# Optimization experiments

Measured on AMD Instinct MI355X. Metric: run time of the kernel, lower is better.

The kernel has to match this reference:

```python
import jax, jax.numpy as jnp
import numpy as np

DEPTH = 2
DIM = 512
FF = 2048
INNER = 32
VOCAB = 8192
B = 2
L = 512
LN_EPS = 1e-5


def _layer_norm(x, g, b):
    m = jnp.mean(x, axis=-1, keepdims=True)
    v = jnp.var(x, axis=-1, keepdims=True)
    return (x - m) * jax.lax.rsqrt(v + LN_EPS) * g + b


def _sioconv_layer(x, wa, wx, v_re, v_im, h0_re, h0_im, w_ol):
    # x: [B, L, DIM] float32
    Bb, Ll, _ = x.shape
    I = v_re.shape[0]
    # complex gate a with magnitude sigmoid(log|a|^2)
    af = (x @ wa.T).reshape(Bb, Ll, I, 2)
    a = jax.lax.complex(af[..., 0], af[..., 1])
    m = jnp.square(af[..., 0]) + jnp.square(af[..., 1])
    a = a * jax.lax.rsqrt(m) * jax.nn.sigmoid(jnp.log(m))  # [B,L,I] complex
    # complex input x with magnitude |x| (x * rsqrt(|x|^2) * |x|^2)
    xf = (x @ wx.T).reshape(Bb, Ll, I, 2)
    xc = jax.lax.complex(xf[..., 0], xf[..., 1])
    mx = jnp.square(xf[..., 0]) + jnp.square(xf[..., 1])
    xc = xc * jax.lax.rsqrt(mx) * mx  # [B,L,I] complex
    # cumulative log-decay products: the original's FFT conv of the upper-
    # triangular a_ln against an all-ones matrix is exactly a cumsum along j.
    a_ln = jnp.log(a)  # [B,L,I]
    ii = jnp.arange(Ll)[:, None]
    jj = jnp.arange(Ll)[None, :]
    tri = jnp.where((jj >= ii)[None, None, :, :],
                    jnp.transpose(a_ln, (0, 2, 1))[:, :, None, :],
                    jnp.zeros((), a_ln.dtype))  # [B,I,L,L]: tri[b,d,i,j]=a_ln[b,j,d] for j>=i
    s = jnp.cumsum(tri, axis=3)
    # c[b,d,i,j] = prod_{t=i..j} a[b,t,d] for j>=i; =1 at j=i-1; 0 below.
    c = jnp.where((jj >= ii - 1)[None, None, :, :], jnp.exp(s), jnp.zeros((), s.dtype))
    V = jax.lax.complex(v_re, v_im)
    Vinv = jnp.linalg.inv(V)
    h0 = jax.lax.complex(h0_re, h0_im)  # [I]
    xct = jnp.transpose(xc, (0, 2, 1))  # [B,I,L]
    x_roll = jnp.roll(xct, 1, axis=2).at[:, :, 0].set(h0[None, :])
    # original builds C[b,l,m,n,o] = V diag(c) V^-1 then einsum; contract lazily:
    y = jnp.einsum('ko,bol->bkl', Vinv, x_roll)  # eigenbasis inputs [B,I,L]
    t = jnp.einsum('bkij,bki->bjk', c, y)        # recurrence in eigenbasis [B,L,I]
    h = jnp.einsum('bjk,nk->bjn', t, V)          # back to state basis [B,L,I]
    h = h.at[:, -1, :].add(xc[:, -1, :])         # last step input (others already in c via j=i-1 band)
    return jnp.real(h) @ w_ol.T


def setup_inputs() -> dict:
    key = jax.random.key(0)
    ks = jax.random.split(key, 16)
    f = lambda k, shp: jax.random.normal(k, shp, dtype=jnp.float32)
    return {
        'x': f(ks[0], (B, L, VOCAB)),
        'w_in': f(ks[1], (DIM, VOCAB)) * VOCAB ** -0.5,
        'b_in': jnp.zeros((DIM,), jnp.float32),
        'ln1_g': jnp.ones((DEPTH, DIM), jnp.float32),
        'ln1_b': jnp.zeros((DEPTH, DIM), jnp.float32),
        'wa': f(ks[2], (DEPTH, 2 * INNER, DIM)) * DIM ** -0.5,
        'wx': f(ks[3], (DEPTH, 2 * INNER, DIM)) * DIM ** -0.5,
        'v_re': f(ks[4], (DEPTH, INNER, INNER)),
        'v_im': f(ks[5], (DEPTH, INNER, INNER)),
        'h0_re': f(ks[6], (DEPTH, INNER)),
        'h0_im': f(ks[7], (DEPTH, INNER)),
        'w_ol': f(ks[8], (DEPTH, DIM, INNER)) * INNER ** -0.5,
        'ln2_g': jnp.ones((DEPTH, DIM), jnp.float32),
        'ln2_b': jnp.zeros((DEPTH, DIM), jnp.float32),
        'w1': f(ks[9], (DEPTH, FF, DIM)) * DIM ** -0.5,
        'b1': jnp.zeros((DEPTH, FF), jnp.float32),
        'w2': f(ks[10], (DEPTH, DIM, FF)) * FF ** -0.5,
        'b2': jnp.zeros((DEPTH, DIM), jnp.float32),
        'lnl_g': jnp.ones((DIM,), jnp.float32),
        'lnl_b': jnp.zeros((DIM,), jnp.float32),
        'w_out': f(ks[11], (VOCAB, DIM)) * DIM ** -0.5,
        'b_out': jnp.zeros((VOCAB,), jnp.float32),
    }


def reference(x, w_in, b_in, ln1_g, ln1_b, wa, wx, v_re, v_im, h0_re, h0_im,
              w_ol, ln2_g, ln2_b, w1, b1, w2, b2, lnl_g, lnl_b, w_out, b_out):
    h = x @ w_in.T + b_in  # [B,L,DIM]
    for d in range(DEPTH):
        r = h
        z = _layer_norm(h, ln1_g[d], ln1_b[d])
        z = _sioconv_layer(z, wa[d], wx[d], v_re[d], v_im[d], h0_re[d], h0_im[d], w_ol[d])
        h = z + r
        r = h
        z = _layer_norm(h, ln2_g[d], ln2_b[d])
        z = jax.nn.silu(z @ w1[d].T + b1[d]) @ w2[d].T + b2[d]
        h = z + r
    h = _layer_norm(h, lnl_g, lnl_b)
    return h @ w_out.T + b_out
```

## Files before the change

### kernel.cpp

```cpp
#include <hip/hip_runtime.h>
#include <stdint.h>

#define DEPTHC 2
#define DIMC   512
#define FFC    2048
#define INNERC 32
#define VOCABC 8192
#define BC     2
#define LC     512
#define NTOK   1024

typedef _Float16 f16;
typedef __attribute__((ext_vector_type(8))) _Float16 f16x8;
typedef __attribute__((ext_vector_type(4))) float f32x4;

__device__ __forceinline__ float2 cmul2(float2 a, float2 b){
    return make_float2(a.x*b.x - a.y*b.y, a.x*b.y + a.y*b.x);
}
__device__ __forceinline__ float2 cadd2(float2 a, float2 b){
    return make_float2(a.x + b.x, a.y + b.y);
}

__device__ __forceinline__ void gl_lds16(const void* g, void* l){
    __builtin_amdgcn_global_load_lds(
        (const __attribute__((address_space(1))) unsigned int*)g,
        (__attribute__((address_space(3))) unsigned int*)l, 16, 0, 0);
}

__global__ __launch_bounds__(256) void k_prep(
    const float* __restrict__ s0, const float* __restrict__ s1,
    const float* __restrict__ s2, const float* __restrict__ s3,
    const float* __restrict__ s4,
    f16* __restrict__ d0, f16* __restrict__ d1, f16* __restrict__ d2,
    f16* __restrict__ d3, f16* __restrict__ d4,
    int n0, int n1, int n2, int n3, int n4,
    const float* __restrict__ v_re, const float* __restrict__ v_im,
    const float* __restrict__ h0re, const float* __restrict__ h0im,
    float2* __restrict__ vinv, float2* __restrict__ h0c)
{
    __shared__ float2 M[32][64];
    if (blockIdx.x < 2){
        const int d = blockIdx.x;
        const int tid = threadIdx.x;
        const int c = tid & 63;
        const int wv = tid >> 6;
        if (tid < 32) h0c[d*32 + tid] = make_float2(h0re[d*32 + tid], h0im[d*32 + tid]);
#pragma unroll
        for (int rr = 0; rr < 8; ++rr){
            int r = wv*8 + rr;
            float re, im;
            if (c < 32){ re = v_re[d*1024 + r*32 + c]; im = v_im[d*1024 + r*32 + c]; }
            else       { re = (c - 32 == r) ? 1.f : 0.f; im = 0.f; }
            M[r][c] = make_float2(re, im);
        }
        __syncthreads();
#pragma unroll 1
        for (int col = 0; col < 32; ++col){
            float2 prow = M[col][c];
            float pvx = __shfl(prow.x, col, 64);
            float pvy = __shfl(prow.y, col, 64);
            float dm = pvx*pvx + pvy*pvy;
            float ir = pvx/dm, ii = -pvy/dm;
            float2 nv = make_float2(prow.x*ir - prow.y*ii, prow.x*ii + prow.y*ir);
#pragma unroll
            for (int rr = 0; rr < 8; ++rr){
                int r = wv*8 + rr;
                if (r == col) continue;
                float2 f  = M[r][col];
                float2 m0 = M[r][c];
                m0.x -= f.x*nv.x - f.y*nv.y;
                m0.y -= f.x*nv.y + f.y*nv.x;
                M[r][c] = m0;
            }
            __syncthreads();
        }
        if (c >= 32){
#pragma unroll
            for (int rr = 0; rr < 8; ++rr){
                int r = wv*8 + rr;
                float2 dv = M[r][r];
                float dm = dv.x*dv.x + dv.y*dv.y;
                float ir = dv.x/dm, ii = -dv.y/dm;
                float2 m0 = M[r][c];
                vinv[d*1024 + r*32 + (c - 32)] =
                    make_float2(m0.x*ir - m0.y*ii, m0.x*ii + m0.y*ir);
            }
        }
        return;
    }
    long long i = ((long long)(blockIdx.x - 2) * 256 + threadIdx.x) * 4;
    const float* s; f16* d;
    if (i < n0){ s = s0; d = d0; }
    else { i -= n0;
        if (i < n1){ s = s1; d = d1; }
        else { i -= n1;
            if (i < n2){ s = s2; d = d2; }
            else { i -= n2;
                if (i < n3){ s = s3; d = d3; }
                else { i -= n3; if (i >= n4) return; s = s4; d = d4; }
            }
        }
    }
    float4 v = *(const float4*)(s + i);
    union { f16 h[4]; float2 f2; } u;
    u.h[0] = (f16)v.x; u.h[1] = (f16)v.y; u.h[2] = (f16)v.z; u.h[3] = (f16)v.w;
    *(float2*)(d + i) = u.f2;
}

template<int MT, int NT, int MODE>
__global__ __launch_bounds__(256) void k_gemmT(
    const f16* __restrict__ A, const f16* __restrict__ Bw,
    void* __restrict__ C, const float* __restrict__ bias,
    int N, int K, int klen, int partStride)
{
    constexpr int RM = MT/32, RN = NT/32;
    __shared__ __align__(16) f16 As[MT*64];
    __shared__ __align__(16) f16 Bs[NT*64];
    const int tid = threadIdx.x;
    const int m0 = blockIdx.y * MT;
    const int n0 = blockIdx.x * NT;
    const int kbeg = blockIdx.z * klen;
    const int l = tid & 63;
    const int w = tid >> 6;
    const int fr = l & 15;
    const int fq = l >> 4;
    const int wm = (w >> 1) * (MT/2);
    const int wn = (w & 1) * (NT/2);
    const f16* gA = A  + (size_t)(m0 + (tid >> 3)) * K + kbeg + (tid & 7) * 8;
    const f16* gB = Bw + (size_t)(n0 + (tid >> 3)) * K + kbeg + (tid & 7) * 8;
    const size_t rowskip = (size_t)32 * K;
    f16* lA = As + tid * 8;
    f16* lB = Bs + tid * 8;
    f32x4 acc[RM][RN];
#pragma unroll
    for (int i = 0; i < RM; ++i)
#pragma unroll
        for (int j = 0; j < RN; ++j)
            acc[i][j] = (f32x4){0.f, 0.f, 0.f, 0.f};
    for (int kk = 0; kk < klen; kk += 64){
        __syncthreads();
#pragma unroll
        for (int i = 0; i < MT/32; ++i) gl_lds16(gA + i*rowskip, lA + i*2048);
#pragma unroll
        for (int i = 0; i < NT/32; ++i) gl_lds16(gB + i*rowskip, lB + i*2048);
        gA += 64; gB += 64;
        __syncthreads();
#pragma unroll
        for (int h = 0; h < 2; ++h){
            f16x8 af[RM], bf[RN];
#pragma unroll
            for (int i = 0; i < RM; ++i) af[i] = *(const f16x8*)(As + (wm + 16*i + fr) * 64 + h*32 + fq * 8);
#pragma unroll
            for (int j = 0; j < RN; ++j) bf[j] = *(const f16x8*)(Bs + (wn + 16*j + fr) * 64 + h*32 + fq * 8);
#pragma unroll
            for (int i = 0; i < RM; ++i)
#pragma unroll
                for (int j = 0; j < RN; ++j)
                    acc[i][j] = __builtin_amdgcn_mfma_f32_16x16x32_f16(af[i], bf[j], acc[i][j], 0, 0, 0);
        }
    }
#pragma unroll
    for (int i = 0; i < RM; ++i)
#pragma unroll
        for (int j = 0; j < RN; ++j)
#pragma unroll
            for (int r = 0; r < 4; ++r){
                int row = m0 + wm + 16*i + fq*4 + r;
                int col = n0 + wn + 16*j + fr;
                if (MODE == 1){
                    ((f16*)C + (size_t)blockIdx.z * partStride)[(size_t)row * N + col] = (f16)acc[i][j][r];
                } else if (MODE == 0){
                    ((float*)C)[(size_t)row * N + col] = acc[i][j][r] + bias[col];
                } else {
                    float v = acc[i][j][r] + bias[col];
                    ((f16*)C)[(size_t)row * N + col] = (f16)(v / (1.f + __expf(-v)));
                }
            }
}

__global__ __launch_bounds__(128) void k_red8_ln(
    const f16* __restrict__ part, const float* __restrict__ bias,
    const float* __restrict__ res, const float* __restrict__ g,
    const float* __restrict__ b, f16* __restrict__ out, int n)
{
    int row = blockIdx.x;
    int tid = threadIdx.x;
    __shared__ float sw[2], qw[2];
    float v[4]; float s = 0.f, q = 0.f;
#pragma unroll
    for (int j = 0; j < 4; ++j){
        int c = tid + 128*j;
        int idx = row*DIMC + c;
        float t = bias[c] + res[idx];
#pragma unroll
        for (int z = 0; z < 8; ++z) t += (float)part[(size_t)z * n + idx];
        v[j] = t; s += t; q += t*t;
    }
    for (int off = 32; off; off >>= 1){ s += __shfl_down(s, off, 64); q += __shfl_down(q, off, 64); }
    if ((tid & 63) == 0){ sw[tid >> 6] = s; qw[tid >> 6] = q; }
    __syncthreads();
    float S = sw[0] + sw[1], Q = qw[0] + qw[1];
    float m = S / DIMC;
    float rstd = rsqrtf(Q / DIMC - m*m + 1e-5f);
#pragma unroll
    for (int j = 0; j < 4; ++j){
        int c = tid + 128*j;
        out[(size_t)row*DIMC + c] = (f16)((v[j] - m)*rstd*g[c] + b[c]);
    }
}

__global__ __launch_bounds__(128) void k_siogate(
    const f16* __restrict__ part, const float* __restrict__ bias0,
    const float* __restrict__ res, float* __restrict__ hout,
    const float* __restrict__ g, const float* __restrict__ b,
    const float* __restrict__ wa, const float* __restrict__ wx,
    float2* __restrict__ a_t, float2* __restrict__ xc)
{
    __shared__ float zs[4][DIMC];
    __shared__ float sc[4][128];
    __shared__ float rs2[2], rq2[2];
    int tid = threadIdx.x;
    int r0 = blockIdx.x * 4;
    for (int gg = 0; gg < 4; ++gg){
        int row = r0 + gg;
        float v[4]; float s = 0.f, q = 0.f;
#pragma unroll
        for (int j = 0; j < 4; ++j){
            int c = tid + 128*j;
            size_t idx = (size_t)row * DIMC + c;
            float t = bias0[c];
            if (res) t += res[idx];
#pragma unroll
            for (int z = 0; z < 8; ++z) t += (float)part[(size_t)z * (NTOK*DIMC) + idx];
            hout[idx] = t;
            v[j] = t; s += t; q += t*t;
        }
        for (int off = 32; off; off >>= 1){ s += __shfl_down(s, off, 64); q += __shfl_down(q, off, 64); }
        if ((tid & 63) == 0){ rs2[tid >> 6] = s; rq2[tid >> 6] = q; }
        __syncthreads();
        float m = (rs2[0] + rs2[1]) / DIMC;
        float var = (rq2[0] + rq2[1]) / DIMC - m*m;
        float rst = rsqrtf(var + 1e-5f);
#pragma unroll
        for (int j = 0; j < 4; ++j){ int c = tid + 128*j; zs[gg][c] = (v[j] - m)*rst*g[c] + b[c]; }
        __syncthreads();
    }
    const float* wrow = (tid < 64) ? (wa + (size_t)tid * DIMC) : (wx + (size_t)(tid - 64) * DIMC);
    float dot[4] = {0.f, 0.f, 0.f, 0.f};
    for (int c = 0; c < DIMC; c += 4){
        float4 wv = *(const float4*)(wrow + c);
#pragma unroll
        for (int gg = 0; gg < 4; ++gg){
            float4 zv = *(const float4*)(&zs[gg][c]);
            dot[gg] += wv.x*zv.x + wv.y*zv.y + wv.z*zv.z + wv.w*zv.w;
        }
    }
#pragma unroll
    for (int gg = 0; gg < 4; ++gg) sc[gg][tid] = dot[gg];
    __syncthreads();
    int gg = tid >> 5, k = tid & 31;
    int row = r0 + gg;
    int bb = row >> 9, t = row & 511;
    float re = sc[gg][2*k], im = sc[gg][2*k + 1];
    float m2 = re*re + im*im;
    float sa = rsqrtf(m2) * (m2 / (1.f + m2));
    a_t[(size_t)(bb*INNERC + k)*LC + t] = make_float2(re*sa, im*sa);
    float xr2 = sc[gg][64 + 2*k], xi2 = sc[gg][64 + 2*k + 1];
    float mx = xr2*xr2 + xi2*xi2;
    float sx = sqrtf(mx);
    xc[(size_t)row*INNERC + k] = make_float2(xr2*sx, xi2*sx);
}

__global__ __launch_bounds__(64) void k_scan(
    const float2* __restrict__ a_t, const float2* __restrict__ xc,
    const float2* __restrict__ vinv, const float2* __restrict__ h0c,
    float2* __restrict__ e)
{
    int bk = blockIdx.x;
    int l = threadIdx.x;
    int bb = bk >> 5, k = bk & 31;
    float2 vrow[32];
#pragma unroll
    for (int o = 0; o < 32; ++o) vrow[o] = vinv[k*32 + o];
    int base = bk * LC + l * 8;
    float2 av[8], wv[8];
#pragma unroll
    for (int j = 0; j < 8; ++j) av[j] = a_t[base + j];
#pragma unroll
    for (int j = 0; j < 8; ++j){
        int t = l*8 + j;
        const float2* src = (t == 0) ? h0c : (xc + (size_t)(bb*LC + t - 1) * INNERC);
        float2 acc = make_float2(0.f, 0.f);
#pragma unroll
        for (int o = 0; o < 32; o += 2){
            float4 qq = *(const float4*)(src + o);
            acc.x += vrow[o].x*qq.x - vrow[o].y*qq.y;
            acc.y += vrow[o].x*qq.y + vrow[o].y*qq.x;
            acc.x += vrow[o+1].x*qq.z - vrow[o+1].y*qq.w;
            acc.y += vrow[o+1].x*qq.w + vrow[o+1].y*qq.z;
        }
        wv[j] = acc;
    }
    float2 A = make_float2(1.f, 0.f), Bc = make_float2(0.f, 0.f);
#pragma unroll
    for (int j = 0; j < 8; ++j){
        Bc = cmul2(av[j], cadd2(Bc, wv[j]));
        A  = cmul2(av[j], A);
    }
    for (int off = 1; off < 64; off <<= 1){
        float Apx = __shfl_up(A.x,  off, 64), Apy = __shfl_up(A.y,  off, 64);
        float Bpx = __shfl_up(Bc.x, off, 64), Bpy = __shfl_up(Bc.y, off, 64);
        if (l >= off){
            float2 Ap = make_float2(Apx, Apy), Bp = make_float2(Bpx, Bpy);
            Bc = cadd2(cmul2(A, Bp), Bc);
            A  = cmul2(A, Ap);
        }
    }
    float ex = __shfl_up(Bc.x, 1, 64), ey = __shfl_up(Bc.y, 1, 64);
    float2 ecur = (l == 0) ? make_float2(0.f, 0.f) : make_float2(ex, ey);
    size_t obase = ((size_t)bb*LC + l*8) * INNERC + k;
#pragma unroll
    for (int j = 0; j < 8; ++j){
        ecur = cmul2(av[j], cadd2(ecur, wv[j]));
        e[obase + (size_t)j * INNERC] = ecur;
    }
}

__global__ __launch_bounds__(128) void k_siout_ln(
    const float2* __restrict__ e, const float2* __restrict__ xc,
    const float* __restrict__ vre, const float* __restrict__ vim,
    const float* __restrict__ wol, const float* __restrict__ res,
    const float* __restrict__ g2, const float* __restrict__ b2,
    float* __restrict__ hout, f16* __restrict__ zout)
{
    int bt = blockIdx.x;
    int tid = threadIdx.x;
    __shared__ float hr[INNERC];
    __shared__ float2 er[INNERC];
    __shared__ float sw[2], qw[2];
    if (tid < 32) er[tid] = e[(size_t)bt*INNERC + tid];
    __syncthreads();
    if (tid < 32){
        const float* vrr = vre + tid*INNERC;
        const float* vir = vim + tid*INNERC;
        float acc = xc[(size_t)bt*INNERC + tid].x;
#pragma unroll
        for (int k2 = 0; k2 < 32; ++k2) acc += vrr[k2]*er[k2].x - vir[k2]*er[k2].y;
        hr[tid] = acc;
    }
    __syncthreads();
    float v[4]; float s = 0.f, q = 0.f;
#pragma unroll
    for (int j = 0; j < 4; ++j){
        int n = tid + 128*j;
        float val = res[(size_t)bt*DIMC + n];
        const float* wr = wol + (size_t)n * INNERC;
#pragma unroll
        for (int i = 0; i < 32; ++i) val += hr[i]*wr[i];
        hout[(size_t)bt*DIMC + n] = val;
        v[j] = val; s += val; q += val*val;
    }
    for (int off = 32; off; off >>= 1){ s += __shfl_down(s, off, 64); q += __shfl_down(q, off, 64); }
    if ((tid & 63) == 0){ sw[tid >> 6] = s; qw[tid >> 6] = q; }
    __syncthreads();
    float S = sw[0] + sw[1], Q = qw[0] + qw[1];
    float m = S / DIMC;
    float rstd = rsqrtf(Q / DIMC - m*m + 1e-5f);
#pragma unroll
    for (int j = 0; j < 4; ++j){
        int n = tid + 128*j;
        zout[(size_t)bt*DIMC + n] = (f16)((v[j] - m)*rstd*g2[n] + b2[n]);
    }
}

extern "C" void kernel_launch(void* const* d_in, const int* in_sizes, int n_in,
                              void* d_out, int out_size, void* d_ws, size_t ws_size,
                              hipStream_t stream)
{
    const float* x     = (const float*)d_in[0];
    const float* w_in  = (const float*)d_in[1];
    const float* b_in  = (const float*)d_in[2];
    const float* ln1_g = (const float*)d_in[3];
    const float* ln1_b = (const float*)d_in[4];
    const float* wa    = (const float*)d_in[5];
    const float* wx    = (const float*)d_in[6];
    const float* v_re  = (const float*)d_in[7];
    const float* v_im  = (const float*)d_in[8];
    const float* h0_re = (const float*)d_in[9];
    const float* h0_im = (const float*)d_in[10];
    const float* w_ol  = (const float*)d_in[11];
    const float* ln2_g = (const float*)d_in[12];
    const float* ln2_b = (const float*)d_in[13];
    const float* w1    = (const float*)d_in[14];
    const float* b1    = (const float*)d_in[15];
    const float* w2    = (const float*)d_in[16];
    const float* b2    = (const float*)d_in[17];
    const float* lnl_g = (const float*)d_in[18];
    const float* lnl_b = (const float*)d_in[19];
    const float* w_out = (const float*)d_in[20];
    const float* b_out = (const float*)d_in[21];

    char* p = (char*)d_ws;
    f16* xb   = (f16*)p;   p += (size_t)NTOK * VOCABC * 2;
    f16* wib  = (f16*)p;   p += (size_t)DIMC * VOCABC * 2;
    f16* wob  = (f16*)p;   p += (size_t)VOCABC * DIMC * 2;
    f16* w1b  = (f16*)p;   p += (size_t)DEPTHC * FFC * DIMC * 2;
    f16* w2b  = (f16*)p;   p += (size_t)DEPTHC * DIMC * FFC * 2;
    float* h1 = (float*)p; p += (size_t)NTOK * DIMC * 4;
    float* h2 = (float*)p; p += (size_t)NTOK * DIMC * 4;
    float* h3 = (float*)p; p += (size_t)NTOK * DIMC * 4;
    f16* zb   = (f16*)p;   p += (size_t)NTOK * DIMC * 2;
    f16* ffb  = (f16*)p;   p += (size_t)NTOK * FFC * 2;
    f16* pbuf = (f16*)p;   p += (size_t)8 * NTOK * DIMC * 2;
    float2* a_t = (float2*)p; p += (size_t)BC * INNERC * LC * 8;
    float2* xc  = (float2*)p; p += (size_t)NTOK * INNERC * 8;
    float2* ev  = (float2*)p; p += (size_t)NTOK * INNERC * 8;
    float2* vinv = (float2*)p; p += (size_t)DEPTHC * INNERC * INNERC * 8;
    float2* h0c  = (float2*)p; p += (size_t)DEPTHC * INNERC * 8;

    {
        const int n0 = NTOK*VOCABC, n1 = DIMC*VOCABC, n2 = DEPTHC*FFC*DIMC,
                  n3 = DEPTHC*DIMC*FFC, n4 = VOCABC*DIMC;
        int blocks = (n0 + n1 + n2 + n3 + n4) / 1024 + 2;
        k_prep<<<blocks, 256, 0, stream>>>(x, w_in, w1, w2, w_out,
                                           xb, wib, w1b, w2b, wob, n0, n1, n2, n3, n4,
                                           v_re, v_im, h0_re, h0_im, vinv, h0c);
    }

    {
        dim3 g(DIMC/128, NTOK/128, 8);
        k_gemmT<128,128,1><<<g, 256, 0, stream>>>(xb, wib, pbuf, nullptr, DIMC, VOCABC, VOCABC/8, NTOK*DIMC);
    }

    for (int d = 0; d < DEPTHC; ++d){
        float* cur = (d == 0) ? h1 : h3;
        float* hb  = h2;
        const float* redBias = (d == 0) ? b_in : (b2 + (d-1)*DIMC);
        const float* redRes  = (d == 0) ? nullptr : h2;
        k_siogate<<<NTOK/4, 128, 0, stream>>>(pbuf, redBias, redRes, cur,
                                              ln1_g + d*DIMC, ln1_b + d*DIMC,
                                              wa + (size_t)d*2*INNERC*DIMC,
                                              wx + (size_t)d*2*INNERC*DIMC, a_t, xc);
        k_scan<<<BC*INNERC, 64, 0, stream>>>(a_t, xc, vinv + d*INNERC*INNERC, h0c + d*INNERC, ev);
        k_siout_ln<<<NTOK, 128, 0, stream>>>(ev, xc, v_re + d*INNERC*INNERC, v_im + d*INNERC*INNERC,
                                             w_ol + (size_t)d*DIMC*INNERC, cur,
                                             ln2_g + d*DIMC, ln2_b + d*DIMC, hb, zb);
        {
            dim3 g(FFC/128, NTOK/64, 1);
            k_gemmT<64,128,2><<<g, 256, 0, stream>>>(zb, w1b + (size_t)d*FFC*DIMC, ffb, b1 + d*FFC,
                                                     FFC, DIMC, DIMC, 0);
        }
        {
            dim3 g(DIMC/128, NTOK/64, 8);
            k_gemmT<64,128,1><<<g, 256, 0, stream>>>(ffb, w2b + (size_t)d*DIMC*FFC, pbuf, nullptr,
                                                     DIMC, FFC, FFC/8, NTOK*DIMC);
        }
    }
    k_red8_ln<<<NTOK, 128, 0, stream>>>(pbuf, b2 + (DEPTHC-1)*DIMC, h2, lnl_g, lnl_b, zb, NTOK*DIMC);
    {
        dim3 g(VOCABC/128, NTOK/128, 1);
        k_gemmT<128,128,0><<<g, 256, 0, stream>>>(zb, wob, (float*)d_out, b_out, VOCABC, DIMC, DIMC, 0);
    }
    (void)in_sizes; (void)n_in; (void)out_size; (void)ws_size;
}
```

Baseline: 378.1 us.

## Move SioConv gate projection onto MFMA GEMM with fused complex-gate epilogue

Replaces the fused LayerNorm-plus-scalar-dot-product gate kernel with a separate LayerNorm kernel followed by an fp16 MFMA GEMM (new MODE 3). The GEMM epilogue pairs real and imaginary lanes via a shuffle and computes the a and x complex gates. The wa/wx weights are converted to fp16 in the prep kernel. The input projection GEMM tile also changes from 128x128 to 64x128 to launch more blocks. This trades an extra launch and round trip through global memory for tensor-core throughput, and gate inputs now go through fp16.

```diff
diff --git a/kernel.cpp b/kernel.cpp
--- a/kernel.cpp
+++ b/kernel.cpp
@@ -31,8 +31,9 @@
     const float* __restrict__ s0, const float* __restrict__ s1,
     const float* __restrict__ s2, const float* __restrict__ s3,
     const float* __restrict__ s4,
+    const float* __restrict__ wa4, const float* __restrict__ wx4,
     f16* __restrict__ d0, f16* __restrict__ d1, f16* __restrict__ d2,
-    f16* __restrict__ d3, f16* __restrict__ d4,
+    f16* __restrict__ d3, f16* __restrict__ d4, f16* __restrict__ wgb,
     int n0, int n1, int n2, int n3, int n4,
     const float* __restrict__ v_re, const float* __restrict__ v_im,
     const float* __restrict__ h0re, const float* __restrict__ h0im,
@@ -97,7 +98,27 @@
             if (i < n2){ s = s2; d = d2; }
             else { i -= n2;
                 if (i < n3){ s = s3; d = d3; }
-                else { i -= n3; if (i >= n4) return; s = s4; d = d4; }
+                else { i -= n3;
+                    if (i < n4){ s = s4; d = d4; }
+                    else {
+                        i -= n4;
+                        if (i >= 131072) return;
+                        const float* gs; f16* gd;
+                        if (i < 65536){
+                            int dd = (int)(i >> 15), rem = (int)(i & 32767);
+                            gs = wa4 + i; gd = wgb + dd*65536 + rem;
+                        } else {
+                            long long e2 = i - 65536;
+                            int dd = (int)(e2 >> 15), rem = (int)(e2 & 32767);
+                            gs = wx4 + e2; gd = wgb + dd*65536 + 32768 + rem;
+                        }
+                        float4 v = *(const float4*)gs;
+                        union { f16 h[4]; float2 f2; } u;
+                        u.h[0] = (f16)v.x; u.h[1] = (f16)v.y; u.h[2] = (f16)v.z; u.h[3] = (f16)v.w;
+                        *(float2*)gd = u.f2;
+                        return;
+                    }
+                }
             }
         }
     }
@@ -111,7 +132,8 @@
 __global__ __launch_bounds__(256) void k_gemmT(
     const f16* __restrict__ A, const f16* __restrict__ Bw,
     void* __restrict__ C, const float* __restrict__ bias,
-    int N, int K, int klen, int partStride)
+    int N, int K, int klen, int partStride,
+    float2* __restrict__ a_tp, float2* __restrict__ xcp)
 {
     constexpr int RM = MT/32, RN = NT/32;
     __shared__ __align__(16) f16 As[MT*64];
@@ -171,17 +193,35 @@
                     ((f16*)C + (size_t)blockIdx.z * partStride)[(size_t)row * N + col] = (f16)acc[i][j][r];
                 } else if (MODE == 0){
                     ((float*)C)[(size_t)row * N + col] = acc[i][j][r] + bias[col];
-                } else {
+                } else if (MODE == 2){
                     float v = acc[i][j][r] + bias[col];
                     ((f16*)C)[(size_t)row * N + col] = (f16)(v / (1.f + __expf(-v)));
+                } else {
+                    float val = acc[i][j][r];
+                    float pv = __shfl_xor(val, 1, 64);
+                    if (!(fr & 1)){
+                        float re = val, im = pv;
+                        int bb = row >> 9, t = row & 511;
+                        float m2 = re*re + im*im;
+                        if (col < 64){
+                            int k = col >> 1;
+                            float sa = rsqrtf(m2) * (m2 / (1.f + m2));
+                            a_tp[(size_t)(bb*INNERC + k)*LC + t] = make_float2(re*sa, im*sa);
+                        } else {
+                            int k = (col - 64) >> 1;
+                            float sx = sqrtf(m2);
+                            xcp[(size_t)row*INNERC + k] = make_float2(re*sx, im*sx);
+                        }
+                    }
                 }
             }
 }
 
-__global__ __launch_bounds__(128) void k_red8_ln(
+__global__ __launch_bounds__(128) void k_ln1(
     const f16* __restrict__ part, const float* __restrict__ bias,
     const float* __restrict__ res, const float* __restrict__ g,
-    const float* __restrict__ b, f16* __restrict__ out, int n)
+    const float* __restrict__ b, f16* __restrict__ out,
+    float* __restrict__ hout, int n)
 {
     int row = blockIdx.x;
     int tid = threadIdx.x;
@@ -191,9 +231,11 @@
     for (int j = 0; j < 4; ++j){
         int c = tid + 128*j;
         int idx = row*DIMC + c;
-        float t = bias[c] + res[idx];
+        float t = bias[c];
+        if (res) t += res[idx];
 #pragma unroll
         for (int z = 0; z < 8; ++z) t += (float)part[(size_t)z * n + idx];
+        if (hout) hout[idx] = t;
         v[j] = t; s += t; q += t*t;
     }
     for (int off = 32; off; off >>= 1){ s += __shfl_down(s, off, 64); q += __shfl_down(q, off, 64); }
@@ -207,68 +249,6 @@
         int c = tid + 128*j;
         out[(size_t)row*DIMC + c] = (f16)((v[j] - m)*rstd*g[c] + b[c]);
     }
-}
-
-__global__ __launch_bounds__(128) void k_siogate(
-    const f16* __restrict__ part, const float* __restrict__ bias0,
-    const float* __restrict__ res, float* __restrict__ hout,
-    const float* __restrict__ g, const float* __restrict__ b,
-    const float* __restrict__ wa, const float* __restrict__ wx,
-    float2* __restrict__ a_t, float2* __restrict__ xc)
-{
-    __shared__ float zs[4][DIMC];
-    __shared__ float sc[4][128];
-    __shared__ float rs2[2], rq2[2];
-    int tid = threadIdx.x;
-    int r0 = blockIdx.x * 4;
-    for (int gg = 0; gg < 4; ++gg){
-        int row = r0 + gg;
-        float v[4]; float s = 0.f, q = 0.f;
-#pragma unroll
-        for (int j = 0; j < 4; ++j){
-            int c = tid + 128*j;
-            size_t idx = (size_t)row * DIMC + c;
-            float t = bias0[c];
-            if (res) t += res[idx];
-#pragma unroll
-            for (int z = 0; z < 8; ++z) t += (float)part[(size_t)z * (NTOK*DIMC) + idx];
-            hout[idx] = t;
-            v[j] = t; s += t; q += t*t;
-        }
-        for (int off = 32; off; off >>= 1){ s += __shfl_down(s, off, 64); q += __shfl_down(q, off, 64); }
-        if ((tid & 63) == 0){ rs2[tid >> 6] = s; rq2[tid >> 6] = q; }
-        __syncthreads();
-        float m = (rs2[0] + rs2[1]) / DIMC;
-        float var = (rq2[0] + rq2[1]) / DIMC - m*m;
-        float rst = rsqrtf(var + 1e-5f);
-#pragma unroll
-        for (int j = 0; j < 4; ++j){ int c = tid + 128*j; zs[gg][c] = (v[j] - m)*rst*g[c] + b[c]; }
-        __syncthreads();
-    }
-    const float* wrow = (tid < 64) ? (wa + (size_t)tid * DIMC) : (wx + (size_t)(tid - 64) * DIMC);
-    float dot[4] = {0.f, 0.f, 0.f, 0.f};
-    for (int c = 0; c < DIMC; c += 4){
-        float4 wv = *(const float4*)(wrow + c);
-#pragma unroll
-        for (int gg = 0; gg < 4; ++gg){
-            float4 zv = *(const float4*)(&zs[gg][c]);
-            dot[gg] += wv.x*zv.x + wv.y*zv.y + wv.z*zv.z + wv.w*zv.w;
-        }
-    }
-#pragma unroll
-    for (int gg = 0; gg < 4; ++gg) sc[gg][tid] = dot[gg];
-    __syncthreads();
-    int gg = tid >> 5, k = tid & 31;
-    int row = r0 + gg;
-    int bb = row >> 9, t = row & 511;
-    float re = sc[gg][2*k], im = sc[gg][2*k + 1];
-    float m2 = re*re + im*im;
-    float sa = rsqrtf(m2) * (m2 / (1.f + m2));
-    a_t[(size_t)(bb*INNERC + k)*LC + t] = make_float2(re*sa, im*sa);
-    float xr2 = sc[gg][64 + 2*k], xi2 = sc[gg][64 + 2*k + 1];
-    float mx = xr2*xr2 + xi2*xi2;
-    float sx = sqrtf(mx);
-    xc[(size_t)row*INNERC + k] = make_float2(xr2*sx, xi2*sx);
 }
 
 __global__ __launch_bounds__(64) void k_scan(
@@ -406,6 +386,7 @@
     f16* wob  = (f16*)p;   p += (size_t)VOCABC * DIMC * 2;
     f16* w1b  = (f16*)p;   p += (size_t)DEPTHC * FFC * DIMC * 2;
     f16* w2b  = (f16*)p;   p += (size_t)DEPTHC * DIMC * FFC * 2;
+    f16* wgb  = (f16*)p;   p += (size_t)DEPTHC * 2*INNERC*2 * DIMC * 2;
     float* h1 = (float*)p; p += (size_t)NTOK * DIMC * 4;
     float* h2 = (float*)p; p += (size_t)NTOK * DIMC * 4;
     float* h3 = (float*)p; p += (size_t)NTOK * DIMC * 4;
@@ -421,15 +402,17 @@
     {
         const int n0 = NTOK*VOCABC, n1 = DIMC*VOCABC, n2 = DEPTHC*FFC*DIMC,
                   n3 = DEPTHC*DIMC*FFC, n4 = VOCABC*DIMC;
-        int blocks = (n0 + n1 + n2 + n3 + n4) / 1024 + 2;
-        k_prep<<<blocks, 256, 0, stream>>>(x, w_in, w1, w2, w_out,
-                                           xb, wib, w1b, w2b, wob, n0, n1, n2, n3, n4,
+        int blocks = (n0 + n1 + n2 + n3 + n4 + 131072) / 1024 + 2;
+        k_prep<<<blocks, 256, 0, stream>>>(x, w_in, w1, w2, w_out, wa, wx,
+                                           xb, wib, w1b, w2b, wob, wgb,
+                                           n0, n1, n2, n3, n4,
                                            v_re, v_im, h0_re, h0_im, vinv, h0c);
     }
 
     {
-        dim3 g(DIMC/128, NTOK/128, 8);
-        k_gemmT<128,128,1><<<g, 256, 0, stream>>>(xb, wib, pbuf, nullptr, DIMC, VOCABC, VOCABC/8, NTOK*DIMC);
+        dim3 g(DIMC/128, NTOK/64, 8);
+        k_gemmT<64,128,1><<<g, 256, 0, stream>>>(xb, wib, pbuf, nullptr, DIMC, VOCABC, VOCABC/8, NTOK*DIMC,
+                                                 nullptr, nullptr);
     }
 
     for (int d = 0; d < DEPTHC; ++d){
@@ -437,10 +420,13 @@
         float* hb  = h2;
         const float* redBias = (d == 0) ? b_in : (b2 + (d-1)*DIMC);
         const float* redRes  = (d == 0) ? nullptr : h2;
-        k_siogate<<<NTOK/4, 128, 0, stream>>>(pbuf, redBias, redRes, cur,
-                                              ln1_g + d*DIMC, ln1_b + d*DIMC,
-                                              wa + (size_t)d*2*INNERC*DIMC,
-                                              wx + (size_t)d*2*INNERC*DIMC, a_t, xc);
+        k_ln1<<<NTOK, 128, 0, stream>>>(pbuf, redBias, redRes,
+                                        ln1_g + d*DIMC, ln1_b + d*DIMC, zb, cur, NTOK*DIMC);
+        {
+            dim3 g(1, NTOK/32, 1);
+            k_gemmT<32,128,3><<<g, 256, 0, stream>>>(zb, wgb + (size_t)d*128*DIMC, nullptr, nullptr,
+                                                     128, DIMC, DIMC, 0, a_t, xc);
+        }
         k_scan<<<BC*INNERC, 64, 0, stream>>>(a_t, xc, vinv + d*INNERC*INNERC, h0c + d*INNERC, ev);
         k_siout_ln<<<NTOK, 128, 0, stream>>>(ev, xc, v_re + d*INNERC*INNERC, v_im + d*INNERC*INNERC,
                                              w_ol + (size_t)d*DIMC*INNERC, cur,
@@ -448,18 +434,19 @@
         {
             dim3 g(FFC/128, NTOK/64, 1);
             k_gemmT<64,128,2><<<g, 256, 0, stream>>>(zb, w1b + (size_t)d*FFC*DIMC, ffb, b1 + d*FFC,
-                                                     FFC, DIMC, DIMC, 0);
+                                                     FFC, DIMC, DIMC, 0, nullptr, nullptr);
         }
         {
             dim3 g(DIMC/128, NTOK/64, 8);
             k_gemmT<64,128,1><<<g, 256, 0, stream>>>(ffb, w2b + (size_t)d*DIMC*FFC, pbuf, nullptr,
-                                                     DIMC, FFC, FFC/8, NTOK*DIMC);
-        }
-    }
-    k_red8_ln<<<NTOK, 128, 0, stream>>>(pbuf, b2 + (DEPTHC-1)*DIMC, h2, lnl_g, lnl_b, zb, NTOK*DIMC);
+                                                     DIMC, FFC, FFC/8, NTOK*DIMC, nullptr, nullptr);
+        }
+    }
+    k_ln1<<<NTOK, 128, 0, stream>>>(pbuf, b2 + (DEPTHC-1)*DIMC, h2, lnl_g, lnl_b, zb, nullptr, NTOK*DIMC);
     {
         dim3 g(VOCABC/128, NTOK/128, 1);
-        k_gemmT<128,128,0><<<g, 256, 0, stream>>>(zb, wob, (float*)d_out, b_out, VOCABC, DIMC, DIMC, 0);
+        k_gemmT<128,128,0><<<g, 256, 0, stream>>>(zb, wob, (float*)d_out, b_out, VOCABC, DIMC, DIMC, 0,
+                                                  nullptr, nullptr);
     }
     (void)in_sizes; (void)n_in; (void)out_size; (void)ws_size;
 }
```

Measured after the change: 337.3 us. 1.12x faster.
